# Kernel tuning notes

Measured on AMD Instinct MI355X. Metric: run time of the kernel, lower is better.

Reference implementation:

```python
import jax, jax.numpy as jnp
import numpy as np

B = 65536   # batch
HS = 8      # max hand size
E = 12      # card embed dim
A = 20      # max actions
KC = 4      # max cards per action (padded with 0)
NH, HD = 4, 3  # MHA heads, head dim (12/4)


def _xavier(k, out_dim, in_dim, gain):
    lim = gain * np.sqrt(6.0 / (in_dim + out_dim))
    return jax.random.uniform(k, (out_dim, in_dim), jnp.float32, -lim, lim)


def setup_inputs() -> dict:
    key = jax.random.key(0)
    ks = jax.random.split(key, 32)
    card_emb = 0.1 * jax.random.normal(ks[0], (54, E), jnp.float32)
    card_emb = card_emb.at[0].set(0.0)  # padding_idx=0
    enemy_emb = 0.1 * jax.random.normal(ks[1], (54, E), jnp.float32)
    enemy_emb = enemy_emb.at[0].set(0.0)
    inp = {
        'hand_cards': jax.random.randint(ks[2], (B, HS), 0, 54),
        'game_state': jax.random.normal(ks[3], (B, 12), jnp.float32),
        'discard_pile_cards': jax.random.uniform(ks[4], (B, 54), jnp.float32),
        'enemy_card': jax.random.randint(ks[5], (B, 1), 0, 54),
        'hand_size': jax.random.randint(ks[6], (B,), 1, HS + 1),
        'action_card_indices': jax.random.randint(ks[7], (A, KC), 0, 54),
        'num_valid_actions': 20,
        'card_emb': card_emb,
        'enemy_emb': enemy_emb,
        'in_w': _xavier(ks[8], 3 * E, E, 0.5),   # MHA in_proj (torch layout [3E,E])
        'in_b': jnp.zeros((3 * E,), jnp.float32),
        'out_w': _xavier(ks[9], E, E, 0.5),
        'out_b': jnp.zeros((E,), jnp.float32),
        'gs_w1': _xavier(ks[10], 64, 12, 0.8), 'gs_b1': jnp.zeros((64,)),
        'gs_w2': _xavier(ks[11], 6, 64, 0.8), 'gs_b2': jnp.zeros((6,)),
        'dp_w1': _xavier(ks[12], 64, 54, 0.8), 'dp_b1': jnp.zeros((64,)),
        'dp_w2': _xavier(ks[13], 6, 64, 0.8), 'dp_b2': jnp.zeros((6,)),
        'ctx_w1': _xavier(ks[14], 128, 36, 0.8), 'ctx_b1': jnp.zeros((128,)),
        'ctx_w2': _xavier(ks[15], 128, 128, 0.8), 'ctx_b2': jnp.zeros((128,)),
        'sc_w1': _xavier(ks[16], 32, 140, 0.8), 'sc_b1': jnp.zeros((32,)),
        'sc_w2': _xavier(ks[17], 1, 32, 0.8), 'sc_b2': jnp.zeros((1,)),
    }
    return inp


def reference(hand_cards, game_state, discard_pile_cards, enemy_card, hand_size,
              action_card_indices, num_valid_actions,
              card_emb, enemy_emb, in_w, in_b, out_w, out_b,
              gs_w1, gs_b1, gs_w2, gs_b2, dp_w1, dp_b1, dp_w2, dp_b2,
              ctx_w1, ctx_b1, ctx_w2, ctx_b2, sc_w1, sc_b1, sc_w2, sc_b2):
    b = hand_cards.shape[0]
    # hand embeddings + self-attention with key padding mask (card 0 = pad)
    he = card_emb[hand_cards]                                  # [B,8,12]
    mask = hand_cards != 0                                     # [B,8]
    qkv = he @ in_w.T + in_b                                   # [B,8,36]
    q, k, v = jnp.split(qkv, 3, axis=-1)
    hsplit = lambda t: t.reshape(b, HS, NH, HD)
    s = jnp.einsum('bqhd,bkhd->bhqk', hsplit(q), hsplit(k)) / np.sqrt(HD)
    s = jnp.where(mask[:, None, None, :], s, -1e9)
    attn = jax.nn.softmax(s, axis=-1)
    att = jnp.einsum('bhqk,bkhd->bqhd', attn, hsplit(v)).reshape(b, HS, E)
    att = att @ out_w.T + out_b                                # [B,8,12]
    lengths = jnp.maximum(hand_size.astype(jnp.float32), 1.0)[:, None]
    hand_ctx = att.sum(axis=1) / lengths                       # [B,12]
    # enemy / game-state / discard encoders (eval mode: dropout off)
    en = enemy_emb[enemy_card[:, 0]]                           # [B,12]
    g = jax.nn.relu(game_state @ gs_w1.T + gs_b1) @ gs_w2.T + gs_b2        # [B,6]
    d = jax.nn.relu(discard_pile_cards @ dp_w1.T + dp_b1) @ dp_w2.T + dp_b2  # [B,6]
    ctx = jnp.concatenate([hand_ctx, en, g, d], axis=-1)       # [B,36]
    ctx = jax.nn.relu(ctx @ ctx_w1.T + ctx_b1) @ ctx_w2.T + ctx_b2         # [B,128]
    # ragged per-action card lists: masked mean of card embeddings
    aemb = card_emb[action_card_indices]                       # [A,K,12]
    am = (action_card_indices != 0).astype(jnp.float32)[..., None]
    cnt = jnp.maximum(am.sum(axis=1), 1.0)
    arep = (aemb * am).sum(axis=1) / cnt                       # [A,12]
    feat = jnp.concatenate([
        jnp.broadcast_to(ctx[:, None, :], (b, A, ctx.shape[-1])),
        jnp.broadcast_to(arep[None], (b, A, E)),
    ], axis=-1)                                                # [B,A,140]
    sc = (jax.nn.relu(feat @ sc_w1.T + sc_b1) @ sc_w2.T + sc_b2)[..., 0]   # [B,A]
    valid = jnp.arange(A) < num_valid_actions
    return jnp.where(valid[None, :], sc, -1e8)
```

## Files before the change

kernel.cpp:

```cpp
#include <hip/hip_runtime.h>
#include <math.h>

#define HS 8
#define E 12
#define NA 20
#define KC 4

typedef float f32x4 __attribute__((ext_vector_type(4)));
typedef short short8 __attribute__((ext_vector_type(8)));

__device__ float g_ET[4 * 54 * 54];
__device__ float g_VT[4 * 54 * 4];
__device__ float g_abias[NA * 32];
__device__ float g_cb1f[128];
__device__ __align__(16) short g_gsB[4 * 64 * 16];
__device__ __align__(16) short g_dpB[8 * 64 * 16];
__device__ __align__(16) short g_ctxB2[40 * 64 * 16];
__device__ __align__(16) short g_WtB[8 * 64 * 16];
__device__ __align__(16) float g_feat[65536 * 32];

__device__ __forceinline__ void split_bf16(float f, short& hi, short& lo) {
    unsigned u = __float_as_uint(f);
    unsigned r = (u + 0x7FFFu + ((u >> 16) & 1u)) >> 16;
    hi = (short)r;
    float fh = __uint_as_float(r << 16);
    unsigned v = __float_as_uint(f - fh);
    unsigned r2 = (v + 0x7FFFu + ((v >> 16) & 1u)) >> 16;
    lo = (short)r2;
}

__device__ __forceinline__ void split8(const float* x, short8& hi, short8& lo) {
#pragma unroll
    for (int j = 0; j < 8; ++j) {
        short h, l;
        split_bf16(x[j], h, l);
        hi[j] = h; lo[j] = l;
    }
}

#define MFMA(a, b, c) __builtin_amdgcn_mfma_f32_16x16x32_bf16(a, b, c, 0, 0, 0)

__device__ __forceinline__ f32x4 mfma3(short8 ah, short8 al, const short* frag, f32x4 c) {
    const short8* bp = (const short8*)frag;
    short8 bh = bp[0], bl = bp[1];
    c = MFMA(ah, bh, c);
    c = MFMA(ah, bl, c);
    c = MFMA(al, bh, c);
    return c;
}

__device__ float wprime(int hid, int k, const float* ctx_w1, const float* out_w,
                        const float* out_b, const float* gs_w2, const float* dp_w2) {
    if (k < 12) {
        float s = 0.f;
        for (int i = 0; i < 12; ++i) s += ctx_w1[hid * 36 + i] * out_w[i * 12 + k];
        return s;
    } else if (k < 24) {
        return ctx_w1[hid * 36 + k];
    } else if (k == 24) {
        float s = 0.f;
        for (int i = 0; i < 12; ++i) s += ctx_w1[hid * 36 + i] * out_b[i];
        return 8.f * s;
    } else if (k < 32) {
        return 0.f;
    } else if (k < 96) {
        int u = k - 32;
        float s = 0.f;
        for (int c = 0; c < 6; ++c) s += ctx_w1[hid * 36 + 24 + c] * gs_w2[c * 64 + u];
        return s;
    } else {
        int u = k - 96;
        float s = 0.f;
        for (int c = 0; c < 6; ++c) s += ctx_w1[hid * 36 + 30 + c] * dp_w2[c * 64 + u];
        return s;
    }
}

__global__ void precompute_kernel(const float* __restrict__ card_emb,
                                  const int* __restrict__ aci,
                                  const float* __restrict__ ctx_w2,
                                  const float* __restrict__ ctx_b2,
                                  const float* __restrict__ sc_w1,
                                  const float* __restrict__ sc_b1,
                                  const float* __restrict__ in_w,
                                  const float* __restrict__ in_b,
                                  const float* __restrict__ ctx_w1,
                                  const float* __restrict__ ctx_b1,
                                  const float* __restrict__ dp_w1,
                                  const float* __restrict__ gs_w1,
                                  const float* __restrict__ gs_w2,
                                  const float* __restrict__ gs_b2,
                                  const float* __restrict__ dp_w2,
                                  const float* __restrict__ dp_b2,
                                  const float* __restrict__ out_w,
                                  const float* __restrict__ out_b) {
    const int O_ET = 11664, O_VT = O_ET + 216, O_GS = O_VT + 2048, O_DP = O_GS + 4096;
    const int O_CX = O_DP + 20480, O_WT = O_CX + 4096, O_AB = O_WT + 640, O_CB = O_AB + 128;
    int t = blockIdx.x * 256 + threadIdx.x;
    if (t < O_ET) {
        int h = t / 2916, rem = t % 2916;
        int c1 = rem / 54, c2 = rem % 54;
        float s = 0.f;
#pragma unroll
        for (int d = 0; d < 3; ++d) {
            float q = in_b[h * 3 + d], k = in_b[12 + h * 3 + d];
            for (int j = 0; j < 12; ++j) {
                q += in_w[(h * 3 + d) * 12 + j] * card_emb[c1 * 12 + j];
                k += in_w[(12 + h * 3 + d) * 12 + j] * card_emb[c2 * 12 + j];
            }
            s += q * k;
        }
        g_ET[t] = expf(s * 0.5773502691896258f);
    } else if (t < O_VT) {
        int t2 = t - O_ET;
        int h = t2 / 54, c = t2 % 54;
#pragma unroll
        for (int d = 0; d < 3; ++d) {
            float v = in_b[24 + h * 3 + d];
            for (int j = 0; j < 12; ++j)
                v += in_w[(24 + h * 3 + d) * 12 + j] * card_emb[c * 12 + j];
            g_VT[t2 * 4 + d] = v;
        }
        g_VT[t2 * 4 + 3] = 1.0f;
    } else if (t < O_GS) {
        int id = t - O_VT;
        int tt = id >> 9, lane = (id >> 3) & 63, j = id & 7;
        int g = lane >> 4, n = lane & 15;
        int k = 8 * g + j, col = 16 * tt + n;
        float wv = (k < 12) ? gs_w1[col * 12 + k] : 0.f;
        short hi, lo;
        split_bf16(wv, hi, lo);
        int base = ((tt << 6) + lane) << 4;
        g_gsB[base + j] = hi;
        g_gsB[base + 8 + j] = lo;
    } else if (t < O_DP) {
        int id = t - O_GS;
        int st = id >> 9, lane = (id >> 3) & 63, j = id & 7;
        int s = st >> 2, tt = st & 3;
        int g = lane >> 4, n = lane & 15;
        int k = 32 * s + 8 * g + j, col = 16 * tt + n;
        float wv = (k < 54) ? dp_w1[col * 54 + k] : 0.f;
        short hi, lo;
        split_bf16(wv, hi, lo);
        int base = ((st << 6) + lane) << 4;
        g_dpB[base + j] = hi;
        g_dpB[base + 8 + j] = lo;
    } else if (t < O_CX) {
        int id = t - O_DP;
        int st = id >> 9, lane = (id >> 3) & 63, j = id & 7;
        int s = st / 8, tt = st % 8;
        int g = lane >> 4, n = lane & 15;
        int k = 32 * s + 8 * g + j, col = 16 * tt + n;
        float wv = wprime(col, k, ctx_w1, out_w, out_b, gs_w2, dp_w2);
        short hi, lo;
        split_bf16(wv, hi, lo);
        int base = ((st << 6) + lane) << 4;
        g_ctxB2[base + j] = hi;
        g_ctxB2[base + 8 + j] = lo;
    } else if (t < O_WT) {
        int id = t - O_CX;
        int st = id >> 9, lane = (id >> 3) & 63, j = id & 7;
        int s = st >> 1, tt = st & 1;
        int g = lane >> 4, n = lane & 15;
        int k = 32 * s + 8 * g + j, col = 16 * tt + n;
        float wv = 0.f;
        for (int i = 0; i < 128; ++i) wv += sc_w1[col * 140 + i] * ctx_w2[i * 128 + k];
        short hi, lo;
        split_bf16(wv, hi, lo);
        int base = ((st << 6) + lane) << 4;
        g_WtB[base + j] = hi;
        g_WtB[base + 8 + j] = lo;
    } else if (t < O_AB) {
        int t2 = t - O_WT;
        int a = t2 >> 5, j = t2 & 31;
        float arep[E];
#pragma unroll
        for (int k2 = 0; k2 < E; ++k2) arep[k2] = 0.f;
        float cnt = 0.f;
#pragma unroll
        for (int c = 0; c < KC; ++c) {
            int idx = aci[a * KC + c];
            if (idx != 0) {
                cnt += 1.f;
#pragma unroll
                for (int k2 = 0; k2 < E; ++k2) arep[k2] += card_emb[idx * E + k2];
            }
        }
        float inv = 1.f / fmaxf(cnt, 1.f);
        float s = sc_b1[j];
#pragma unroll
        for (int k2 = 0; k2 < E; ++k2) s += sc_w1[j * 140 + 128 + k2] * (arep[k2] * inv);
        for (int i = 0; i < 128; ++i) s += sc_w1[j * 140 + i] * ctx_b2[i];
        g_abias[t2] = s;
    } else if (t < O_CB) {
        int hid = t - O_AB;
        float s = ctx_b1[hid];
        for (int c = 0; c < 6; ++c) {
            s += ctx_w1[hid * 36 + 24 + c] * gs_b2[c];
            s += ctx_w1[hid * 36 + 30 + c] * dp_b2[c];
        }
        g_cb1f[hid] = s;
    }
}

__global__ __launch_bounds__(1024) void featA_kernel(
    const int* __restrict__ hand_cards, const int* __restrict__ enemy_card,
    const int* __restrict__ hand_size, const float* __restrict__ enemy_emb) {
    __shared__ float sET[4 * 54 * 54];
    __shared__ __align__(16) float4 sV[4 * 54];
    __shared__ float sEN[54 * 12];

    int tid = threadIdx.x;
    for (int i = tid; i < 11664; i += 1024) sET[i] = g_ET[i];
    for (int i = tid; i < 864; i += 1024) ((float*)sV)[i] = g_VT[i];
    for (int i = tid; i < 648; i += 1024) sEN[i] = enemy_emb[i];
    __syncthreads();

    int q = tid & 3;
    int el = tid >> 2;
    int b = blockIdx.x * 256 + el;

    int hc[HS];
    {
        const int4* hp = (const int4*)(hand_cards + (size_t)b * HS);
        int4 h0 = hp[0], h1 = hp[1];
        hc[0] = h0.x; hc[1] = h0.y; hc[2] = h0.z; hc[3] = h0.w;
        hc[4] = h1.x; hc[5] = h1.y; hc[6] = h1.z; hc[7] = h1.w;
    }
    int ec = enemy_card[b];

    float4 vv[HS];
#pragma unroll
    for (int k = 0; k < HS; ++k) {
        float4 v = sV[q * 54 + hc[k]];
        if (hc[k] == 0) v = make_float4(0.f, 0.f, 0.f, 0.f);
        vv[k] = v;
    }

    const float* eb = sET + q * 2916;
    float a0 = 0.f, a1 = 0.f, a2 = 0.f;
#pragma unroll
    for (int p = 0; p < HS; ++p) {
        const float* er = eb + hc[p] * 54;
        float n0 = 0.f, n1 = 0.f, n2 = 0.f, nw = 0.f;
#pragma unroll
        for (int k = 0; k < HS; ++k) {
            float e = er[hc[k]];
            n0 += e * vv[k].x;
            n1 += e * vv[k].y;
            n2 += e * vv[k].z;
            nw += e * vv[k].w;
        }
        float rw = 1.f / fmaxf(nw, 1e-30f);
        a0 += n0 * rw; a1 += n1 * rw; a2 += n2 * rw;
    }
    float invlen = 1.f / fmaxf((float)hand_size[b], 1.f);
    float* fr = g_feat + (size_t)b * 32;
    fr[3 * q + 0] = a0 * invlen;
    fr[3 * q + 1] = a1 * invlen;
    fr[3 * q + 2] = a2 * invlen;
    fr[12 + 3 * q + 0] = sEN[ec * 12 + 3 * q + 0];
    fr[12 + 3 * q + 1] = sEN[ec * 12 + 3 * q + 1];
    fr[12 + 3 * q + 2] = sEN[ec * 12 + 3 * q + 2];
    if (q == 0) fr[24] = invlen;
}

#define FENCE() do { asm volatile("s_waitcnt lgkmcnt(0)" ::: "memory"); \
                     __builtin_amdgcn_sched_barrier(0); } while (0)

__global__ __launch_bounds__(256) void scoreB_kernel(
    const float* __restrict__ game_state, const float* __restrict__ discard,
    const int* __restrict__ num_valid, const float* __restrict__ gs_b1,
    const float* __restrict__ dp_b1, const float* __restrict__ sc_w2,
    const float* __restrict__ sc_b2, float* __restrict__ out) {
    __shared__ __align__(16) float sA[4 * 16 * 132];
    __shared__ __align__(16) float sAB[NA * 36];
    __shared__ __align__(16) float sW2[32];
    __shared__ float sCB[128];
    __shared__ float sGSB[64];
    __shared__ float sDPB[64];

    int tid = threadIdx.x;
    for (int i = tid; i < NA * 36; i += 256) {
        int a = i / 36, c = i % 36;
        sAB[i] = (c < 32) ? g_abias[a * 32 + c] : 0.f;
    }
    if (tid >= 160 && tid < 192) sW2[tid - 160] = sc_w2[tid - 160];
    if (tid < 128) sCB[tid] = g_cb1f[tid];
    if (tid >= 192 && tid < 256) sGSB[tid - 192] = gs_b1[tid - 192];
    if (tid >= 128 && tid < 160) { sDPB[tid - 128] = dp_b1[tid - 128]; sDPB[tid - 96] = dp_b1[tid - 96]; }
    __syncthreads();

    int lane = tid & 63;
    int w = tid >> 6;
    int n = lane & 15, g = lane >> 4;
    size_t b2 = (size_t)blockIdx.x * 64 + (w << 4) + n;
    float* SA = sA + w * 2112;

    {
        float xg[8];
#pragma unroll
        for (int j = 0; j < 8; ++j) {
            int k = 8 * g + j;
            xg[j] = (k < 12) ? game_state[b2 * 12 + k] : 0.f;
        }
        short8 xh, xl;
        split8(xg, xh, xl);
        f32x4 gacc[4];
#pragma unroll
        for (int t = 0; t < 4; ++t) {
            float bv = sGSB[16 * t + n];
            f32x4 cc = {bv, bv, bv, bv};
            gacc[t] = mfma3(xh, xl, &g_gsB[((t << 6) + lane) << 4], cc);
        }
#pragma unroll
        for (int t = 0; t < 4; ++t)
#pragma unroll
            for (int r = 0; r < 4; ++r)
                SA[(4 * g + r) * 132 + 16 * t + n] = fmaxf(gacc[t][r], 0.f);
    }
    {
        const float* drow = discard + b2 * 54;
        float xa[8], xb[8];
        {
            const float2* p = (const float2*)(drow + 8 * g);
            float2 v0 = p[0], v1 = p[1], v2 = p[2], v3 = p[3];
            xa[0] = v0.x; xa[1] = v0.y; xa[2] = v1.x; xa[3] = v1.y;
            xa[4] = v2.x; xa[5] = v2.y; xa[6] = v3.x; xa[7] = v3.y;
        }
#pragma unroll
        for (int j = 0; j < 8; ++j) {
            int k = 32 + 8 * g + j;
            xb[j] = (k < 54) ? drow[k] : 0.f;
        }
        short8 ah0, al0, ah1, al1;
        split8(xa, ah0, al0);
        split8(xb, ah1, al1);
        f32x4 dacc[4];
#pragma unroll
        for (int t = 0; t < 4; ++t) {
            float bv = sDPB[16 * t + n];
            f32x4 cc = {bv, bv, bv, bv};
            cc = mfma3(ah0, al0, &g_dpB[((t << 6) + lane) << 4], cc);
            cc = mfma3(ah1, al1, &g_dpB[(((4 + t) << 6) + lane) << 4], cc);
            dacc[t] = cc;
        }
#pragma unroll
        for (int t = 0; t < 4; ++t)
#pragma unroll
            for (int r = 0; r < 4; ++r)
                SA[(4 * g + r) * 132 + 64 + 16 * t + n] = fmaxf(dacc[t][r], 0.f);
    }
    FENCE();

    f32x4 cacc[8];
#pragma unroll
    for (int tt = 0; tt < 8; ++tt) {
        float bv = sCB[16 * tt + n];
        f32x4 cc = {bv, bv, bv, bv};
        cacc[tt] = cc;
    }
    {
        const float4* fp = (const float4*)(g_feat + b2 * 32 + 8 * g);
        float4 f0 = fp[0], f1 = fp[1];
        float ca[8] = {f0.x, f0.y, f0.z, f0.w, f1.x, f1.y, f1.z, f1.w};
        short8 ah, al;
        split8(ca, ah, al);
#pragma unroll
        for (int tt = 0; tt < 8; ++tt)
            cacc[tt] = mfma3(ah, al, &g_ctxB2[((tt << 6) + lane) << 4], cacc[tt]);
    }
#pragma unroll
    for (int s = 1; s < 5; ++s) {
        const float4* ap = (const float4*)&SA[n * 132 + 32 * (s - 1) + 8 * g];
        float4 a0 = ap[0], a1 = ap[1];
        float ca[8] = {a0.x, a0.y, a0.z, a0.w, a1.x, a1.y, a1.z, a1.w};
        short8 ah, al;
        split8(ca, ah, al);
#pragma unroll
        for (int tt = 0; tt < 8; ++tt)
            cacc[tt] = mfma3(ah, al, &g_ctxB2[(((s * 8 + tt) << 6) + lane) << 4], cacc[tt]);
    }
    FENCE();
#pragma unroll
    for (int tt = 0; tt < 8; ++tt)
#pragma unroll
        for (int r = 0; r < 4; ++r)
            SA[(4 * g + r) * 132 + 16 * tt + n] = fmaxf(cacc[tt][r], 0.f);
    FENCE();

    f32x4 uacc[2];
    {
        f32x4 z = {0.f, 0.f, 0.f, 0.f};
        uacc[0] = z; uacc[1] = z;
    }
#pragma unroll
    for (int s = 0; s < 4; ++s) {
        const float4* ap = (const float4*)&SA[n * 132 + 32 * s + 8 * g];
        float4 a0 = ap[0], a1 = ap[1];
        float ha[8] = {a0.x, a0.y, a0.z, a0.w, a1.x, a1.y, a1.z, a1.w};
        short8 ah, al;
        split8(ha, ah, al);
#pragma unroll
        for (int t2 = 0; t2 < 2; ++t2)
            uacc[t2] = mfma3(ah, al, &g_WtB[(((s * 2 + t2) << 6) + lane) << 4], uacc[t2]);
    }
    FENCE();
#pragma unroll
    for (int t2 = 0; t2 < 2; ++t2)
#pragma unroll
        for (int r = 0; r < 4; ++r)
            SA[(4 * g + r) * 132 + 16 * t2 + n] = uacc[t2][r];
    FENCE();

    {
        float uu[32];
        {
            const float4* up = (const float4*)&SA[n * 132];
#pragma unroll
            for (int j8 = 0; j8 < 8; ++j8) {
                float4 v = up[j8];
                uu[4 * j8 + 0] = v.x; uu[4 * j8 + 1] = v.y;
                uu[4 * j8 + 2] = v.z; uu[4 * j8 + 3] = v.w;
            }
        }
        int nva = num_valid[0];
        float sb2 = sc_b2[0];
#pragma unroll
        for (int t = 0; t < 5; ++t) {
            int a = g * 5 + t;
            const float4* ab = (const float4*)&sAB[a * 36];
            float s = sb2;
#pragma unroll
            for (int j8 = 0; j8 < 8; ++j8) {
                float4 av = ab[j8];
                float4 wv = ((const float4*)sW2)[j8];
                s += wv.x * fmaxf(uu[4 * j8 + 0] + av.x, 0.f);
                s += wv.y * fmaxf(uu[4 * j8 + 1] + av.y, 0.f);
                s += wv.z * fmaxf(uu[4 * j8 + 2] + av.z, 0.f);
                s += wv.w * fmaxf(uu[4 * j8 + 3] + av.w, 0.f);
            }
            out[b2 * NA + a] = (a < nva) ? s : -1.0e8f;
        }
    }
}

extern "C" void kernel_launch(void* const* d_in, const int* in_sizes, int n_in,
                              void* d_out, int out_size, void* d_ws, size_t ws_size,
                              hipStream_t stream) {
    const int* hand_cards = (const int*)d_in[0];
    const float* game_state = (const float*)d_in[1];
    const float* discard = (const float*)d_in[2];
    const int* enemy_card = (const int*)d_in[3];
    const int* hand_size = (const int*)d_in[4];
    const int* aci = (const int*)d_in[5];
    const int* num_valid = (const int*)d_in[6];
    const float* card_emb = (const float*)d_in[7];
    const float* enemy_emb = (const float*)d_in[8];
    const float* in_w = (const float*)d_in[9];
    const float* in_b = (const float*)d_in[10];
    const float* out_w = (const float*)d_in[11];
    const float* out_b = (const float*)d_in[12];
    const float* gs_w1 = (const float*)d_in[13];
    const float* gs_b1 = (const float*)d_in[14];
    const float* gs_w2 = (const float*)d_in[15];
    const float* gs_b2 = (const float*)d_in[16];
    const float* dp_w1 = (const float*)d_in[17];
    const float* dp_b1 = (const float*)d_in[18];
    const float* dp_w2 = (const float*)d_in[19];
    const float* dp_b2 = (const float*)d_in[20];
    const float* ctx_w1 = (const float*)d_in[21];
    const float* ctx_b1 = (const float*)d_in[22];
    const float* ctx_w2 = (const float*)d_in[23];
    const float* ctx_b2 = (const float*)d_in[24];
    const float* sc_w1 = (const float*)d_in[25];
    const float* sc_b1 = (const float*)d_in[26];
    const float* sc_w2 = (const float*)d_in[27];
    const float* sc_b2 = (const float*)d_in[28];

    int B = in_sizes[0] / HS;

    precompute_kernel<<<170, 256, 0, stream>>>(
        card_emb, aci, ctx_w2, ctx_b2, sc_w1, sc_b1, in_w, in_b, ctx_w1, ctx_b1,
        dp_w1, gs_w1, gs_w2, gs_b2, dp_w2, dp_b2, out_w, out_b);
    featA_kernel<<<B / 256, 1024, 0, stream>>>(hand_cards, enemy_card, hand_size,
                                               enemy_emb);
    scoreB_kernel<<<B / 64, 256, 0, stream>>>(game_state, discard, num_valid,
                                              gs_b1, dp_b1, sc_w2, sc_b2,
                                              (float*)d_out);
}
```

Baseline: 56.97 us.

## Unfold gs/dp second layers, process two row tiles per wave in scoreB

Stops folding gs_w2/dp_w2 into the ctx first-layer weights, which was a 160-wide K dimension. Instead the 64→6 projections are computed explicitly with FMAs plus cross-lane shuffles, shrinking the ctx MFMA input to K=64. Each wave now handles 32 rows (two 16-row tiles), so every B-fragment load is reused across both tiles. The grid is halved to compensate. bf16 splitting switches to the library conversion intrinsic. The cost is more registers and LDS per block, plus extra shuffle work.

```diff
diff --git a/kernel.cpp b/kernel.cpp
--- a/kernel.cpp
+++ b/kernel.cpp
@@ -1,4 +1,5 @@
 #include <hip/hip_runtime.h>
+#include <hip/hip_bf16.h>
 #include <math.h>
 
 #define HS 8
@@ -12,23 +13,20 @@
 __device__ float g_ET[4 * 54 * 54];
 __device__ float g_VT[4 * 54 * 4];
 __device__ float g_abias[NA * 32];
-__device__ float g_cb1f[128];
 __device__ __align__(16) short g_gsB[4 * 64 * 16];
 __device__ __align__(16) short g_dpB[8 * 64 * 16];
-__device__ __align__(16) short g_ctxB2[40 * 64 * 16];
+__device__ __align__(16) short g_ctxB[16 * 64 * 16];
 __device__ __align__(16) short g_WtB[8 * 64 * 16];
 __device__ __align__(16) float g_feat[65536 * 32];
 
+__device__ __forceinline__ short bfh(float f) {
+    return (short)__bfloat16_as_ushort(__float2bfloat16(f));
+}
 __device__ __forceinline__ void split_bf16(float f, short& hi, short& lo) {
-    unsigned u = __float_as_uint(f);
-    unsigned r = (u + 0x7FFFu + ((u >> 16) & 1u)) >> 16;
-    hi = (short)r;
-    float fh = __uint_as_float(r << 16);
-    unsigned v = __float_as_uint(f - fh);
-    unsigned r2 = (v + 0x7FFFu + ((v >> 16) & 1u)) >> 16;
-    lo = (short)r2;
-}
-
+    hi = bfh(f);
+    float fh = __uint_as_float(((unsigned)(unsigned short)hi) << 16);
+    lo = bfh(f - fh);
+}
 __device__ __forceinline__ void split8(const float* x, short8& hi, short8& lo) {
 #pragma unroll
     for (int j = 0; j < 8; ++j) {
@@ -40,17 +38,16 @@
 
 #define MFMA(a, b, c) __builtin_amdgcn_mfma_f32_16x16x32_bf16(a, b, c, 0, 0, 0)
 
-__device__ __forceinline__ f32x4 mfma3(short8 ah, short8 al, const short* frag, f32x4 c) {
-    const short8* bp = (const short8*)frag;
-    short8 bh = bp[0], bl = bp[1];
+__device__ __forceinline__ f32x4 mfma3v(short8 ah, short8 al, short8 bh, short8 bl,
+                                        f32x4 c) {
     c = MFMA(ah, bh, c);
     c = MFMA(ah, bl, c);
     c = MFMA(al, bh, c);
     return c;
 }
 
-__device__ float wprime(int hid, int k, const float* ctx_w1, const float* out_w,
-                        const float* out_b, const float* gs_w2, const float* dp_w2) {
+__device__ float ctxw(int hid, int k, const float* ctx_w1, const float* out_w,
+                      const float* out_b) {
     if (k < 12) {
         float s = 0.f;
         for (int i = 0; i < 12; ++i) s += ctx_w1[hid * 36 + i] * out_w[i * 12 + k];
@@ -63,17 +60,10 @@
         return 8.f * s;
     } else if (k < 32) {
         return 0.f;
-    } else if (k < 96) {
-        int u = k - 32;
-        float s = 0.f;
-        for (int c = 0; c < 6; ++c) s += ctx_w1[hid * 36 + 24 + c] * gs_w2[c * 64 + u];
-        return s;
-    } else {
-        int u = k - 96;
-        float s = 0.f;
-        for (int c = 0; c < 6; ++c) s += ctx_w1[hid * 36 + 30 + c] * dp_w2[c * 64 + u];
-        return s;
-    }
+    } else if (k < 44) {
+        return ctx_w1[hid * 36 + 24 + (k - 32)];
+    }
+    return 0.f;
 }
 
 __global__ void precompute_kernel(const float* __restrict__ card_emb,
@@ -85,17 +75,12 @@
                                   const float* __restrict__ in_w,
                                   const float* __restrict__ in_b,
                                   const float* __restrict__ ctx_w1,
-                                  const float* __restrict__ ctx_b1,
                                   const float* __restrict__ dp_w1,
                                   const float* __restrict__ gs_w1,
-                                  const float* __restrict__ gs_w2,
-                                  const float* __restrict__ gs_b2,
-                                  const float* __restrict__ dp_w2,
-                                  const float* __restrict__ dp_b2,
                                   const float* __restrict__ out_w,
                                   const float* __restrict__ out_b) {
     const int O_ET = 11664, O_VT = O_ET + 216, O_GS = O_VT + 2048, O_DP = O_GS + 4096;
-    const int O_CX = O_DP + 20480, O_WT = O_CX + 4096, O_AB = O_WT + 640, O_CB = O_AB + 128;
+    const int O_CX = O_DP + 8192, O_WT = O_CX + 4096, O_AB = O_WT + 640;
     int t = blockIdx.x * 256 + threadIdx.x;
     if (t < O_ET) {
         int h = t / 2916, rem = t % 2916;
@@ -148,15 +133,15 @@
     } else if (t < O_CX) {
         int id = t - O_DP;
         int st = id >> 9, lane = (id >> 3) & 63, j = id & 7;
-        int s = st / 8, tt = st % 8;
+        int s = st >> 3, tt = st & 7;
         int g = lane >> 4, n = lane & 15;
-        int k = 32 * s + 8 * g + j, col = 16 * tt + n;
-        float wv = wprime(col, k, ctx_w1, out_w, out_b, gs_w2, dp_w2);
+        int k = 32 * s + 8 * g + j, hid = 16 * tt + n;
+        float wv = ctxw(hid, k, ctx_w1, out_w, out_b);
         short hi, lo;
         split_bf16(wv, hi, lo);
         int base = ((st << 6) + lane) << 4;
-        g_ctxB2[base + j] = hi;
-        g_ctxB2[base + 8 + j] = lo;
+        g_ctxB[base + j] = hi;
+        g_ctxB[base + 8 + j] = lo;
     } else if (t < O_WT) {
         int id = t - O_CX;
         int st = id >> 9, lane = (id >> 3) & 63, j = id & 7;
@@ -192,14 +177,6 @@
         for (int k2 = 0; k2 < E; ++k2) s += sc_w1[j * 140 + 128 + k2] * (arep[k2] * inv);
         for (int i = 0; i < 128; ++i) s += sc_w1[j * 140 + i] * ctx_b2[i];
         g_abias[t2] = s;
-    } else if (t < O_CB) {
-        int hid = t - O_AB;
-        float s = ctx_b1[hid];
-        for (int c = 0; c < 6; ++c) {
-            s += ctx_w1[hid * 36 + 24 + c] * gs_b2[c];
-            s += ctx_w1[hid * 36 + 30 + c] * dp_b2[c];
-        }
-        g_cb1f[hid] = s;
     }
 }
 
@@ -271,11 +248,16 @@
 __global__ __launch_bounds__(256) void scoreB_kernel(
     const float* __restrict__ game_state, const float* __restrict__ discard,
     const int* __restrict__ num_valid, const float* __restrict__ gs_b1,
-    const float* __restrict__ dp_b1, const float* __restrict__ sc_w2,
-    const float* __restrict__ sc_b2, float* __restrict__ out) {
-    __shared__ __align__(16) float sA[4 * 16 * 132];
+    const float* __restrict__ dp_b1, const float* __restrict__ gs_w2,
+    const float* __restrict__ dp_w2, const float* __restrict__ gs_b2,
+    const float* __restrict__ dp_b2, const float* __restrict__ ctx_b1,
+    const float* __restrict__ sc_w2, const float* __restrict__ sc_b2,
+    float* __restrict__ out) {
+    __shared__ __align__(16) float sU[4 * 4224];
     __shared__ __align__(16) float sAB[NA * 36];
     __shared__ __align__(16) float sW2[32];
+    __shared__ __align__(16) float sGS2T[64 * 12];
+    __shared__ __align__(16) float sDPW2T[64 * 12];
     __shared__ float sCB[128];
     __shared__ float sGSB[64];
     __shared__ float sDPB[64];
@@ -285,138 +267,253 @@
         int a = i / 36, c = i % 36;
         sAB[i] = (c < 32) ? g_abias[a * 32 + c] : 0.f;
     }
-    if (tid >= 160 && tid < 192) sW2[tid - 160] = sc_w2[tid - 160];
-    if (tid < 128) sCB[tid] = g_cb1f[tid];
-    if (tid >= 192 && tid < 256) sGSB[tid - 192] = gs_b1[tid - 192];
-    if (tid >= 128 && tid < 160) { sDPB[tid - 128] = dp_b1[tid - 128]; sDPB[tid - 96] = dp_b1[tid - 96]; }
+    for (int i = tid; i < 768; i += 256) {
+        int r = i / 12, c = i % 12;
+        sGS2T[i] = (c < 6) ? gs_w2[c * 64 + r] : 0.f;
+        sDPW2T[i] = (c < 6) ? dp_w2[c * 64 + r] : 0.f;
+    }
+    if (tid < 32) sW2[tid] = sc_w2[tid];
+    if (tid >= 32 && tid < 160) sCB[tid - 32] = ctx_b1[tid - 32];
+    if (tid >= 160 && tid < 224) sGSB[tid - 160] = gs_b1[tid - 160];
+    if (tid >= 192 && tid < 256) sDPB[tid - 192] = dp_b1[tid - 192];
+    for (int i = tid; i < 4 * 640; i += 256) {
+        int w2 = i / 640;
+        sU[w2 * 4224 + (i % 640)] = 0.f;
+    }
     __syncthreads();
 
     int lane = tid & 63;
     int w = tid >> 6;
     int n = lane & 15, g = lane >> 4;
-    size_t b2 = (size_t)blockIdx.x * 64 + (w << 4) + n;
-    float* SA = sA + w * 2112;
-
+    size_t eb0 = (size_t)blockIdx.x * 128 + (w << 5);
+    float* SW = sU + w * 4224;
+    float gb2 = (n < 6) ? gs_b2[n] : 0.f;
+    float db2 = (n < 6) ? dp_b2[n] : 0.f;
+
+    f32x4 gacc[2][4], dacc[2][4];
     {
-        float xg[8];
-#pragma unroll
-        for (int j = 0; j < 8; ++j) {
-            int k = 8 * g + j;
-            xg[j] = (k < 12) ? game_state[b2 * 12 + k] : 0.f;
-        }
-        short8 xh, xl;
-        split8(xg, xh, xl);
-        f32x4 gacc[4];
+        short8 gah[2], gal[2], dah0[2], dal0[2], dah1[2], dal1[2];
+#pragma unroll
+        for (int tau = 0; tau < 2; ++tau) {
+            size_t bE = eb0 + 16 * tau + n;
+            float xg[8];
+#pragma unroll
+            for (int j = 0; j < 8; ++j) {
+                int k = 8 * g + j;
+                xg[j] = (k < 12) ? game_state[bE * 12 + k] : 0.f;
+            }
+            split8(xg, gah[tau], gal[tau]);
+            const float* drow = discard + bE * 54;
+            float xa[8], xb[8];
+            {
+                const float2* p = (const float2*)(drow + 8 * g);
+                float2 v0 = p[0], v1 = p[1], v2 = p[2], v3 = p[3];
+                xa[0] = v0.x; xa[1] = v0.y; xa[2] = v1.x; xa[3] = v1.y;
+                xa[4] = v2.x; xa[5] = v2.y; xa[6] = v3.x; xa[7] = v3.y;
+            }
+#pragma unroll
+            for (int j = 0; j < 8; ++j) {
+                int k = 32 + 8 * g + j;
+                xb[j] = (k < 54) ? drow[k] : 0.f;
+            }
+            split8(xa, dah0[tau], dal0[tau]);
+            split8(xb, dah1[tau], dal1[tau]);
+        }
 #pragma unroll
         for (int t = 0; t < 4; ++t) {
+            const short8* bp = (const short8*)&g_gsB[((t << 6) + lane) << 4];
+            short8 bh = bp[0], bl = bp[1];
             float bv = sGSB[16 * t + n];
-            f32x4 cc = {bv, bv, bv, bv};
-            gacc[t] = mfma3(xh, xl, &g_gsB[((t << 6) + lane) << 4], cc);
-        }
-#pragma unroll
-        for (int t = 0; t < 4; ++t)
-#pragma unroll
-            for (int r = 0; r < 4; ++r)
-                SA[(4 * g + r) * 132 + 16 * t + n] = fmaxf(gacc[t][r], 0.f);
-    }
-    {
-        const float* drow = discard + b2 * 54;
-        float xa[8], xb[8];
-        {
-            const float2* p = (const float2*)(drow + 8 * g);
-            float2 v0 = p[0], v1 = p[1], v2 = p[2], v3 = p[3];
-            xa[0] = v0.x; xa[1] = v0.y; xa[2] = v1.x; xa[3] = v1.y;
-            xa[4] = v2.x; xa[5] = v2.y; xa[6] = v3.x; xa[7] = v3.y;
-        }
-#pragma unroll
-        for (int j = 0; j < 8; ++j) {
-            int k = 32 + 8 * g + j;
-            xb[j] = (k < 54) ? drow[k] : 0.f;
-        }
-        short8 ah0, al0, ah1, al1;
-        split8(xa, ah0, al0);
-        split8(xb, ah1, al1);
-        f32x4 dacc[4];
+#pragma unroll
+            for (int tau = 0; tau < 2; ++tau) {
+                f32x4 cc = {bv, bv, bv, bv};
+                gacc[tau][t] = mfma3v(gah[tau], gal[tau], bh, bl, cc);
+            }
+        }
 #pragma unroll
         for (int t = 0; t < 4; ++t) {
+            const short8* b0 = (const short8*)&g_dpB[((t << 6) + lane) << 4];
+            short8 b0h = b0[0], b0l = b0[1];
+            const short8* b1 = (const short8*)&g_dpB[(((4 + t) << 6) + lane) << 4];
+            short8 b1h = b1[0], b1l = b1[1];
             float bv = sDPB[16 * t + n];
-            f32x4 cc = {bv, bv, bv, bv};
-            cc = mfma3(ah0, al0, &g_dpB[((t << 6) + lane) << 4], cc);
-            cc = mfma3(ah1, al1, &g_dpB[(((4 + t) << 6) + lane) << 4], cc);
-            dacc[t] = cc;
-        }
-#pragma unroll
-        for (int t = 0; t < 4; ++t)
-#pragma unroll
-            for (int r = 0; r < 4; ++r)
-                SA[(4 * g + r) * 132 + 64 + 16 * t + n] = fmaxf(dacc[t][r], 0.f);
+#pragma unroll
+            for (int tau = 0; tau < 2; ++tau) {
+                f32x4 cc = {bv, bv, bv, bv};
+                cc = mfma3v(dah0[tau], dal0[tau], b0h, b0l, cc);
+                dacc[tau][t] = mfma3v(dah1[tau], dal1[tau], b1h, b1l, cc);
+            }
+        }
+    }
+
+#pragma unroll
+    for (int tau = 0; tau < 2; ++tau) {
+        float pg[4][6], pd[4][6];
+#pragma unroll
+        for (int r = 0; r < 4; ++r)
+#pragma unroll
+            for (int c = 0; c < 6; ++c) { pg[r][c] = 0.f; pd[r][c] = 0.f; }
+#pragma unroll
+        for (int t = 0; t < 4; ++t) {
+            const float* wg = &sGS2T[(16 * t + n) * 12];
+            float4 wga = *(const float4*)wg;
+            float2 wgb = *(const float2*)(wg + 4);
+            const float* wd = &sDPW2T[(16 * t + n) * 12];
+            float4 wda = *(const float4*)wd;
+            float2 wdb = *(const float2*)(wd + 4);
+#pragma unroll
+            for (int r = 0; r < 4; ++r) {
+                float hg = fmaxf(gacc[tau][t][r], 0.f);
+                float hd = fmaxf(dacc[tau][t][r], 0.f);
+                pg[r][0] += hg * wga.x; pg[r][1] += hg * wga.y; pg[r][2] += hg * wga.z;
+                pg[r][3] += hg * wga.w; pg[r][4] += hg * wgb.x; pg[r][5] += hg * wgb.y;
+                pd[r][0] += hd * wda.x; pd[r][1] += hd * wda.y; pd[r][2] += hd * wda.z;
+                pd[r][3] += hd * wda.w; pd[r][4] += hd * wdb.x; pd[r][5] += hd * wdb.y;
+            }
+        }
+#pragma unroll
+        for (int r = 0; r < 4; ++r)
+#pragma unroll
+            for (int c = 0; c < 6; ++c) {
+                float v = pg[r][c];
+                v += __shfl_xor(v, 1, 64);
+                v += __shfl_xor(v, 2, 64);
+                v += __shfl_xor(v, 4, 64);
+                v += __shfl_xor(v, 8, 64);
+                pg[r][c] = v;
+                float u = pd[r][c];
+                u += __shfl_xor(u, 1, 64);
+                u += __shfl_xor(u, 2, 64);
+                u += __shfl_xor(u, 4, 64);
+                u += __shfl_xor(u, 8, 64);
+                pd[r][c] = u;
+            }
+        if (n < 6) {
+#pragma unroll
+            for (int r = 0; r < 4; ++r) {
+                int e = 16 * tau + 4 * g + r;
+                float gv = pg[r][0];
+                gv = (n == 1) ? pg[r][1] : gv; gv = (n == 2) ? pg[r][2] : gv;
+                gv = (n == 3) ? pg[r][3] : gv; gv = (n == 4) ? pg[r][4] : gv;
+                gv = (n == 5) ? pg[r][5] : gv;
+                float dv = pd[r][0];
+                dv = (n == 1) ? pd[r][1] : dv; dv = (n == 2) ? pd[r][2] : dv;
+                dv = (n == 3) ? pd[r][3] : dv; dv = (n == 4) ? pd[r][4] : dv;
+                dv = (n == 5) ? pd[r][5] : dv;
+                SW[e * 20 + n] = gv + gb2;
+                SW[e * 20 + 6 + n] = dv + db2;
+            }
+        }
     }
     FENCE();
 
-    f32x4 cacc[8];
+    f32x4 cacc[2][8];
 #pragma unroll
     for (int tt = 0; tt < 8; ++tt) {
         float bv = sCB[16 * tt + n];
-        f32x4 cc = {bv, bv, bv, bv};
-        cacc[tt] = cc;
+#pragma unroll
+        for (int tau = 0; tau < 2; ++tau) {
+            f32x4 cc = {bv, bv, bv, bv};
+            cacc[tau][tt] = cc;
+        }
     }
     {
-        const float4* fp = (const float4*)(g_feat + b2 * 32 + 8 * g);
-        float4 f0 = fp[0], f1 = fp[1];
-        float ca[8] = {f0.x, f0.y, f0.z, f0.w, f1.x, f1.y, f1.z, f1.w};
-        short8 ah, al;
-        split8(ca, ah, al);
+        short8 ah[2], al[2];
+#pragma unroll
+        for (int tau = 0; tau < 2; ++tau) {
+            size_t bE = eb0 + 16 * tau + n;
+            const float4* fp = (const float4*)(g_feat + bE * 32 + 8 * g);
+            float4 f0 = fp[0], f1 = fp[1];
+            float ca[8] = {f0.x, f0.y, f0.z, f0.w, f1.x, f1.y, f1.z, f1.w};
+            split8(ca, ah[tau], al[tau]);
+        }
+#pragma unroll
+        for (int tt = 0; tt < 8; ++tt) {
+            const short8* bp = (const short8*)&g_ctxB[((tt << 6) + lane) << 4];
+            short8 bh = bp[0], bl = bp[1];
+#pragma unroll
+            for (int tau = 0; tau < 2; ++tau)
+                cacc[tau][tt] = mfma3v(ah[tau], al[tau], bh, bl, cacc[tau][tt]);
+        }
+#pragma unroll
+        for (int tau = 0; tau < 2; ++tau) {
+            if (g < 2) {
+                int e = 16 * tau + n;
+                float xb[8];
+#pragma unroll
+                for (int j2 = 0; j2 < 4; ++j2) {
+                    float2 v = *(const float2*)&SW[e * 20 + 8 * g + 2 * j2];
+                    xb[2 * j2] = v.x;
+                    xb[2 * j2 + 1] = v.y;
+                }
+                split8(xb, ah[tau], al[tau]);
+            } else {
+                short8 zz = {0, 0, 0, 0, 0, 0, 0, 0};
+                ah[tau] = zz; al[tau] = zz;
+            }
+        }
+#pragma unroll
+        for (int tt = 0; tt < 8; ++tt) {
+            const short8* bp = (const short8*)&g_ctxB[(((8 + tt) << 6) + lane) << 4];
+            short8 bh = bp[0], bl = bp[1];
+#pragma unroll
+            for (int tau = 0; tau < 2; ++tau)
+                cacc[tau][tt] = mfma3v(ah[tau], al[tau], bh, bl, cacc[tau][tt]);
+        }
+    }
+    FENCE();
+
+#pragma unroll
+    for (int tau = 0; tau < 2; ++tau)
 #pragma unroll
         for (int tt = 0; tt < 8; ++tt)
-            cacc[tt] = mfma3(ah, al, &g_ctxB2[((tt << 6) + lane) << 4], cacc[tt]);
-    }
-#pragma unroll
-    for (int s = 1; s < 5; ++s) {
-        const float4* ap = (const float4*)&SA[n * 132 + 32 * (s - 1) + 8 * g];
-        float4 a0 = ap[0], a1 = ap[1];
-        float ca[8] = {a0.x, a0.y, a0.z, a0.w, a1.x, a1.y, a1.z, a1.w};
-        short8 ah, al;
-        split8(ca, ah, al);
-#pragma unroll
-        for (int tt = 0; tt < 8; ++tt)
-            cacc[tt] = mfma3(ah, al, &g_ctxB2[(((s * 8 + tt) << 6) + lane) << 4], cacc[tt]);
-    }
+#pragma unroll
+            for (int r = 0; r < 4; ++r)
+                SW[(16 * tau + 4 * g + r) * 132 + 16 * tt + n] =
+                    fmaxf(cacc[tau][tt][r], 0.f);
     FENCE();
-#pragma unroll
-    for (int tt = 0; tt < 8; ++tt)
-#pragma unroll
-        for (int r = 0; r < 4; ++r)
-            SA[(4 * g + r) * 132 + 16 * tt + n] = fmaxf(cacc[tt][r], 0.f);
-    FENCE();
-
-    f32x4 uacc[2];
+
+    f32x4 uacc[2][2];
     {
         f32x4 z = {0.f, 0.f, 0.f, 0.f};
-        uacc[0] = z; uacc[1] = z;
+        uacc[0][0] = z; uacc[0][1] = z; uacc[1][0] = z; uacc[1][1] = z;
     }
 #pragma unroll
     for (int s = 0; s < 4; ++s) {
-        const float4* ap = (const float4*)&SA[n * 132 + 32 * s + 8 * g];
-        float4 a0 = ap[0], a1 = ap[1];
-        float ha[8] = {a0.x, a0.y, a0.z, a0.w, a1.x, a1.y, a1.z, a1.w};
-        short8 ah, al;
-        split8(ha, ah, al);
+        short8 ah[2], al[2];
+#pragma unroll
+        for (int tau = 0; tau < 2; ++tau) {
+            const float4* ap = (const float4*)&SW[(16 * tau + n) * 132 + 32 * s + 8 * g];
+            float4 a0 = ap[0], a1 = ap[1];
+            float ha[8] = {a0.x, a0.y, a0.z, a0.w, a1.x, a1.y, a1.z, a1.w};
+            split8(ha, ah[tau], al[tau]);
+        }
+#pragma unroll
+        for (int t2 = 0; t2 < 2; ++t2) {
+            const short8* bp = (const short8*)&g_WtB[(((s * 2 + t2) << 6) + lane) << 4];
+            short8 bh = bp[0], bl = bp[1];
+#pragma unroll
+            for (int tau = 0; tau < 2; ++tau)
+                uacc[tau][t2] = mfma3v(ah[tau], al[tau], bh, bl, uacc[tau][t2]);
+        }
+    }
+    FENCE();
+
+#pragma unroll
+    for (int tau = 0; tau < 2; ++tau)
 #pragma unroll
         for (int t2 = 0; t2 < 2; ++t2)
-            uacc[t2] = mfma3(ah, al, &g_WtB[(((s * 2 + t2) << 6) + lane) << 4], uacc[t2]);
-    }
+#pragma unroll
+            for (int r = 0; r < 4; ++r)
+                SW[(16 * tau + 4 * g + r) * 132 + 16 * t2 + n] = uacc[tau][t2][r];
     FENCE();
-#pragma unroll
-    for (int t2 = 0; t2 < 2; ++t2)
-#pragma unroll
-        for (int r = 0; r < 4; ++r)
-            SA[(4 * g + r) * 132 + 16 * t2 + n] = uacc[t2][r];
-    FENCE();
-
-    {
+    int nva = num_valid[0];
+    float sb2 = sc_b2[0];
+#pragma unroll
+    for (int tau = 0; tau < 2; ++tau) {
         float uu[32];
         {
-            const float4* up = (const float4*)&SA[n * 132];
+            const float4* up = (const float4*)&SW[(16 * tau + n) * 132];
 #pragma unroll
             for (int j8 = 0; j8 < 8; ++j8) {
                 float4 v = up[j8];
@@ -424,8 +521,7 @@
                 uu[4 * j8 + 2] = v.z; uu[4 * j8 + 3] = v.w;
             }
         }
-        int nva = num_valid[0];
-        float sb2 = sc_b2[0];
+        size_t bE = eb0 + 16 * tau + n;
 #pragma unroll
         for (int t = 0; t < 5; ++t) {
             int a = g * 5 + t;
@@ -440,7 +536,7 @@
                 s += wv.z * fmaxf(uu[4 * j8 + 2] + av.z, 0.f);
                 s += wv.w * fmaxf(uu[4 * j8 + 3] + av.w, 0.f);
             }
-            out[b2 * NA + a] = (a < nva) ? s : -1.0e8f;
+            out[bE * NA + a] = (a < nva) ? s : -1.0e8f;
         }
     }
 }
@@ -480,12 +576,12 @@
 
     int B = in_sizes[0] / HS;
 
-    precompute_kernel<<<170, 256, 0, stream>>>(
-        card_emb, aci, ctx_w2, ctx_b2, sc_w1, sc_b1, in_w, in_b, ctx_w1, ctx_b1,
-        dp_w1, gs_w1, gs_w2, gs_b2, dp_w2, dp_b2, out_w, out_b);
+    precompute_kernel<<<121, 256, 0, stream>>>(
+        card_emb, aci, ctx_w2, ctx_b2, sc_w1, sc_b1, in_w, in_b, ctx_w1,
+        dp_w1, gs_w1, out_w, out_b);
     featA_kernel<<<B / 256, 1024, 0, stream>>>(hand_cards, enemy_card, hand_size,
                                                enemy_emb);
-    scoreB_kernel<<<B / 64, 256, 0, stream>>>(game_state, discard, num_valid,
-                                              gs_b1, dp_b1, sc_w2, sc_b2,
-                                              (float*)d_out);
-}
+    scoreB_kernel<<<B / 128, 256, 0, stream>>>(
+        game_state, discard, num_valid, gs_b1, dp_b1, gs_w2, dp_w2, gs_b2, dp_b2,
+        ctx_b1, sc_w2, sc_b2, (float*)d_out);
+}
```

Result: slower. 74.17 us (+30.2%).

## Split fused scoring kernel into three GEMM kernels with global bf16 intermediates

Applied to the files above, without the earlier changes.

Breaks the single fused scoreB kernel into gemmA (game-state and discard first layers), gemmB (context layer 1) and gemmC (final projection and scoring). The intermediate activations are written to large transposed global buffers as packed hi/lo bf16 pairs. Each kernel stages its weight fragments in shared memory instead of reading them from global. This is meant to cut per-block LDS pressure and improve weight reuse, at the cost of two extra launches and roughly 64MB of extra global write and read traffic per intermediate buffer.

```diff
diff --git a/kernel.cpp b/kernel.cpp
--- a/kernel.cpp
+++ b/kernel.cpp
@@ -1,4 +1,5 @@
 #include <hip/hip_runtime.h>
+#include <hip/hip_bf16.h>
 #include <math.h>
 
 #define HS 8
@@ -18,17 +19,17 @@
 __device__ __align__(16) short g_ctxB2[40 * 64 * 16];
 __device__ __align__(16) short g_WtB[8 * 64 * 16];
 __device__ __align__(16) float g_feat[65536 * 32];
-
+__device__ __align__(16) unsigned g_h1T[128 * 65536];
+__device__ __align__(16) unsigned g_h2T[128 * 65536];
+
+__device__ __forceinline__ short bfh(float f) {
+    return (short)__bfloat16_as_ushort(__float2bfloat16(f));
+}
 __device__ __forceinline__ void split_bf16(float f, short& hi, short& lo) {
-    unsigned u = __float_as_uint(f);
-    unsigned r = (u + 0x7FFFu + ((u >> 16) & 1u)) >> 16;
-    hi = (short)r;
-    float fh = __uint_as_float(r << 16);
-    unsigned v = __float_as_uint(f - fh);
-    unsigned r2 = (v + 0x7FFFu + ((v >> 16) & 1u)) >> 16;
-    lo = (short)r2;
-}
-
+    hi = bfh(f);
+    float fh = __uint_as_float(((unsigned)(unsigned short)hi) << 16);
+    lo = bfh(f - fh);
+}
 __device__ __forceinline__ void split8(const float* x, short8& hi, short8& lo) {
 #pragma unroll
     for (int j = 0; j < 8; ++j) {
@@ -37,12 +38,16 @@
         hi[j] = h; lo[j] = l;
     }
 }
+__device__ __forceinline__ unsigned packsp(float f) {
+    short h, l;
+    split_bf16(f, h, l);
+    return (((unsigned)(unsigned short)h) << 16) | (unsigned)(unsigned short)l;
+}
 
 #define MFMA(a, b, c) __builtin_amdgcn_mfma_f32_16x16x32_bf16(a, b, c, 0, 0, 0)
 
-__device__ __forceinline__ f32x4 mfma3(short8 ah, short8 al, const short* frag, f32x4 c) {
-    const short8* bp = (const short8*)frag;
-    short8 bh = bp[0], bl = bp[1];
+__device__ __forceinline__ f32x4 mfma3v(short8 ah, short8 al, short8 bh, short8 bl,
+                                        f32x4 c) {
     c = MFMA(ah, bh, c);
     c = MFMA(ah, bl, c);
     c = MFMA(al, bh, c);
@@ -150,8 +155,8 @@
         int st = id >> 9, lane = (id >> 3) & 63, j = id & 7;
         int s = st / 8, tt = st % 8;
         int g = lane >> 4, n = lane & 15;
-        int k = 32 * s + 8 * g + j, col = 16 * tt + n;
-        float wv = wprime(col, k, ctx_w1, out_w, out_b, gs_w2, dp_w2);
+        int k = 32 * s + 8 * g + j, hid = 16 * tt + n;
+        float wv = wprime(hid, k, ctx_w1, out_w, out_b, gs_w2, dp_w2);
         short hi, lo;
         split_bf16(wv, hi, lo);
         int base = ((st << 6) + lane) << 4;
@@ -265,62 +270,37 @@
     if (q == 0) fr[24] = invlen;
 }
 
-#define FENCE() do { asm volatile("s_waitcnt lgkmcnt(0)" ::: "memory"); \
-                     __builtin_amdgcn_sched_barrier(0); } while (0)
-
-__global__ __launch_bounds__(256) void scoreB_kernel(
+#define FENCE() asm volatile("s_waitcnt lgkmcnt(0)" ::: "memory")
+
+__global__ __launch_bounds__(256) void gemmA_kernel(
     const float* __restrict__ game_state, const float* __restrict__ discard,
-    const int* __restrict__ num_valid, const float* __restrict__ gs_b1,
-    const float* __restrict__ dp_b1, const float* __restrict__ sc_w2,
-    const float* __restrict__ sc_b2, float* __restrict__ out) {
-    __shared__ __align__(16) float sA[4 * 16 * 132];
-    __shared__ __align__(16) float sAB[NA * 36];
-    __shared__ __align__(16) float sW2[32];
-    __shared__ float sCB[128];
-    __shared__ float sGSB[64];
-    __shared__ float sDPB[64];
+    const float* __restrict__ gs_b1, const float* __restrict__ dp_b1) {
+    __shared__ __align__(16) short sGs[4 * 64 * 16];
+    __shared__ __align__(16) short sDp[8 * 64 * 16];
+    __shared__ float sGSB[64], sDPB[64];
 
     int tid = threadIdx.x;
-    for (int i = tid; i < NA * 36; i += 256) {
-        int a = i / 36, c = i % 36;
-        sAB[i] = (c < 32) ? g_abias[a * 32 + c] : 0.f;
-    }
-    if (tid >= 160 && tid < 192) sW2[tid - 160] = sc_w2[tid - 160];
-    if (tid < 128) sCB[tid] = g_cb1f[tid];
-    if (tid >= 192 && tid < 256) sGSB[tid - 192] = gs_b1[tid - 192];
-    if (tid >= 128 && tid < 160) { sDPB[tid - 128] = dp_b1[tid - 128]; sDPB[tid - 96] = dp_b1[tid - 96]; }
+    for (int i = tid; i < 512; i += 256) ((int4*)sGs)[i] = ((const int4*)g_gsB)[i];
+    for (int i = tid; i < 1024; i += 256) ((int4*)sDp)[i] = ((const int4*)g_dpB)[i];
+    if (tid < 64) sGSB[tid] = gs_b1[tid];
+    if (tid >= 64 && tid < 128) sDPB[tid - 64] = dp_b1[tid - 64];
     __syncthreads();
 
     int lane = tid & 63;
-    int w = tid >> 6;
     int n = lane & 15, g = lane >> 4;
-    size_t b2 = (size_t)blockIdx.x * 64 + (w << 4) + n;
-    float* SA = sA + w * 2112;
-
+    size_t eb = (size_t)blockIdx.x * 64 + ((tid >> 6) << 4);
+    size_t bE = eb + n;
+
+    short8 gah, gal, dah0, dal0, dah1, dal1;
     {
         float xg[8];
 #pragma unroll
         for (int j = 0; j < 8; ++j) {
             int k = 8 * g + j;
-            xg[j] = (k < 12) ? game_state[b2 * 12 + k] : 0.f;
-        }
-        short8 xh, xl;
-        split8(xg, xh, xl);
-        f32x4 gacc[4];
-#pragma unroll
-        for (int t = 0; t < 4; ++t) {
-            float bv = sGSB[16 * t + n];
-            f32x4 cc = {bv, bv, bv, bv};
-            gacc[t] = mfma3(xh, xl, &g_gsB[((t << 6) + lane) << 4], cc);
-        }
-#pragma unroll
-        for (int t = 0; t < 4; ++t)
-#pragma unroll
-            for (int r = 0; r < 4; ++r)
-                SA[(4 * g + r) * 132 + 16 * t + n] = fmaxf(gacc[t][r], 0.f);
-    }
-    {
-        const float* drow = discard + b2 * 54;
+            xg[j] = (k < 12) ? game_state[bE * 12 + k] : 0.f;
+        }
+        split8(xg, gah, gal);
+        const float* drow = discard + bE * 54;
         float xa[8], xb[8];
         {
             const float2* p = (const float2*)(drow + 8 * g);
@@ -333,61 +313,128 @@
             int k = 32 + 8 * g + j;
             xb[j] = (k < 54) ? drow[k] : 0.f;
         }
-        short8 ah0, al0, ah1, al1;
-        split8(xa, ah0, al0);
-        split8(xb, ah1, al1);
-        f32x4 dacc[4];
-#pragma unroll
-        for (int t = 0; t < 4; ++t) {
-            float bv = sDPB[16 * t + n];
+        split8(xa, dah0, dal0);
+        split8(xb, dah1, dal1);
+    }
+#pragma unroll
+    for (int tt = 0; tt < 4; ++tt) {
+        const short8* bp = (const short8*)&sGs[((tt << 6) + lane) << 4];
+        float bv = sGSB[16 * tt + n];
+        f32x4 cc = {bv, bv, bv, bv};
+        cc = mfma3v(gah, gal, bp[0], bp[1], cc);
+        uint4 v;
+        v.x = packsp(fmaxf(cc[0], 0.f));
+        v.y = packsp(fmaxf(cc[1], 0.f));
+        v.z = packsp(fmaxf(cc[2], 0.f));
+        v.w = packsp(fmaxf(cc[3], 0.f));
+        *(uint4*)(g_h1T + (size_t)(16 * tt + n) * 65536 + eb + 4 * g) = v;
+    }
+#pragma unroll
+    for (int tt = 0; tt < 4; ++tt) {
+        const short8* b0 = (const short8*)&sDp[((tt << 6) + lane) << 4];
+        const short8* b1 = (const short8*)&sDp[(((4 + tt) << 6) + lane) << 4];
+        float bv = sDPB[16 * tt + n];
+        f32x4 cc = {bv, bv, bv, bv};
+        cc = mfma3v(dah0, dal0, b0[0], b0[1], cc);
+        cc = mfma3v(dah1, dal1, b1[0], b1[1], cc);
+        uint4 v;
+        v.x = packsp(fmaxf(cc[0], 0.f));
+        v.y = packsp(fmaxf(cc[1], 0.f));
+        v.z = packsp(fmaxf(cc[2], 0.f));
+        v.w = packsp(fmaxf(cc[3], 0.f));
+        *(uint4*)(g_h1T + (size_t)(64 + 16 * tt + n) * 65536 + eb + 4 * g) = v;
+    }
+}
+
+__global__ __launch_bounds__(256) void gemmB_kernel() {
+    __shared__ __align__(16) short sCx[40 * 64 * 16];
+    __shared__ float sCB[128];
+
+    int tid = threadIdx.x;
+    for (int i = tid; i < 5120; i += 256) ((int4*)sCx)[i] = ((const int4*)g_ctxB2)[i];
+    if (tid < 128) sCB[tid] = g_cb1f[tid];
+    __syncthreads();
+
+    int lane = tid & 63;
+    int n = lane & 15, g = lane >> 4;
+    size_t base = (size_t)blockIdx.x * 256 + ((tid >> 6) << 6);
+
+#pragma unroll
+    for (int t = 0; t < 4; ++t) {
+        size_t eb = base + t * 16;
+        size_t bE = eb + n;
+        f32x4 cacc[8];
+#pragma unroll
+        for (int tt = 0; tt < 8; ++tt) {
+            float bv = sCB[16 * tt + n];
             f32x4 cc = {bv, bv, bv, bv};
-            cc = mfma3(ah0, al0, &g_dpB[((t << 6) + lane) << 4], cc);
-            cc = mfma3(ah1, al1, &g_dpB[(((4 + t) << 6) + lane) << 4], cc);
-            dacc[t] = cc;
-        }
-#pragma unroll
-        for (int t = 0; t < 4; ++t)
-#pragma unroll
-            for (int r = 0; r < 4; ++r)
-                SA[(4 * g + r) * 132 + 64 + 16 * t + n] = fmaxf(dacc[t][r], 0.f);
-    }
-    FENCE();
-
-    f32x4 cacc[8];
-#pragma unroll
-    for (int tt = 0; tt < 8; ++tt) {
-        float bv = sCB[16 * tt + n];
-        f32x4 cc = {bv, bv, bv, bv};
-        cacc[tt] = cc;
-    }
-    {
-        const float4* fp = (const float4*)(g_feat + b2 * 32 + 8 * g);
-        float4 f0 = fp[0], f1 = fp[1];
-        float ca[8] = {f0.x, f0.y, f0.z, f0.w, f1.x, f1.y, f1.z, f1.w};
-        short8 ah, al;
-        split8(ca, ah, al);
-#pragma unroll
-        for (int tt = 0; tt < 8; ++tt)
-            cacc[tt] = mfma3(ah, al, &g_ctxB2[((tt << 6) + lane) << 4], cacc[tt]);
-    }
-#pragma unroll
-    for (int s = 1; s < 5; ++s) {
-        const float4* ap = (const float4*)&SA[n * 132 + 32 * (s - 1) + 8 * g];
-        float4 a0 = ap[0], a1 = ap[1];
-        float ca[8] = {a0.x, a0.y, a0.z, a0.w, a1.x, a1.y, a1.z, a1.w};
-        short8 ah, al;
-        split8(ca, ah, al);
-#pragma unroll
-        for (int tt = 0; tt < 8; ++tt)
-            cacc[tt] = mfma3(ah, al, &g_ctxB2[(((s * 8 + tt) << 6) + lane) << 4], cacc[tt]);
-    }
-    FENCE();
-#pragma unroll
-    for (int tt = 0; tt < 8; ++tt)
-#pragma unroll
-        for (int r = 0; r < 4; ++r)
-            SA[(4 * g + r) * 132 + 16 * tt + n] = fmaxf(cacc[tt][r], 0.f);
-    FENCE();
+            cacc[tt] = cc;
+        }
+        {
+            const float4* fp = (const float4*)(g_feat + bE * 32 + 8 * g);
+            float4 f0 = fp[0], f1 = fp[1];
+            float fx[8] = {f0.x, f0.y, f0.z, f0.w, f1.x, f1.y, f1.z, f1.w};
+            short8 ah, al;
+            split8(fx, ah, al);
+#pragma unroll
+            for (int tt = 0; tt < 8; ++tt) {
+                const short8* bp = (const short8*)&sCx[((tt << 6) + lane) << 4];
+                cacc[tt] = mfma3v(ah, al, bp[0], bp[1], cacc[tt]);
+            }
+        }
+#pragma unroll
+        for (int s = 1; s < 5; ++s) {
+            unsigned va[8];
+#pragma unroll
+            for (int j = 0; j < 8; ++j)
+                va[j] = g_h1T[(size_t)((s - 1) * 32 + 8 * g + j) * 65536 + bE];
+            short8 ah, al;
+#pragma unroll
+            for (int j = 0; j < 8; ++j) {
+                ah[j] = (short)(va[j] >> 16);
+                al[j] = (short)(va[j] & 0xffffu);
+            }
+#pragma unroll
+            for (int tt = 0; tt < 8; ++tt) {
+                const short8* bp = (const short8*)&sCx[(((s * 8 + tt) << 6) + lane) << 4];
+                cacc[tt] = mfma3v(ah, al, bp[0], bp[1], cacc[tt]);
+            }
+        }
+#pragma unroll
+        for (int tt = 0; tt < 8; ++tt) {
+            uint4 v;
+            v.x = packsp(fmaxf(cacc[tt][0], 0.f));
+            v.y = packsp(fmaxf(cacc[tt][1], 0.f));
+            v.z = packsp(fmaxf(cacc[tt][2], 0.f));
+            v.w = packsp(fmaxf(cacc[tt][3], 0.f));
+            *(uint4*)(g_h2T + (size_t)(16 * tt + n) * 65536 + eb + 4 * g) = v;
+        }
+    }
+}
+
+__global__ __launch_bounds__(256) void gemmC_kernel(
+    const int* __restrict__ num_valid, const float* __restrict__ sc_w2,
+    const float* __restrict__ sc_b2, float* __restrict__ out) {
+    __shared__ __align__(16) short sWt[8 * 64 * 16];
+    __shared__ __align__(16) float sAB[NA * 36];
+    __shared__ __align__(16) float sW2[32];
+    __shared__ __align__(16) float sT[4 * 16 * 36];
+
+    int tid = threadIdx.x;
+    for (int i = tid; i < 1024; i += 256) ((int4*)sWt)[i] = ((const int4*)g_WtB)[i];
+    for (int i = tid; i < NA * 36; i += 256) {
+        int a = i / 36, c = i % 36;
+        sAB[i] = (c < 32) ? g_abias[a * 32 + c] : 0.f;
+    }
+    if (tid < 32) sW2[tid] = sc_w2[tid];
+    __syncthreads();
+
+    int lane = tid & 63;
+    int w = tid >> 6;
+    int n = lane & 15, g = lane >> 4;
+    size_t eb = (size_t)blockIdx.x * 64 + (w << 4);
+    size_t bE = eb + n;
+    float* SW = sT + w * 576;
 
     f32x4 uacc[2];
     {
@@ -396,27 +443,32 @@
     }
 #pragma unroll
     for (int s = 0; s < 4; ++s) {
-        const float4* ap = (const float4*)&SA[n * 132 + 32 * s + 8 * g];
-        float4 a0 = ap[0], a1 = ap[1];
-        float ha[8] = {a0.x, a0.y, a0.z, a0.w, a1.x, a1.y, a1.z, a1.w};
+        unsigned va[8];
+#pragma unroll
+        for (int j = 0; j < 8; ++j)
+            va[j] = g_h2T[(size_t)(32 * s + 8 * g + j) * 65536 + bE];
         short8 ah, al;
-        split8(ha, ah, al);
-#pragma unroll
-        for (int t2 = 0; t2 < 2; ++t2)
-            uacc[t2] = mfma3(ah, al, &g_WtB[(((s * 2 + t2) << 6) + lane) << 4], uacc[t2]);
-    }
+#pragma unroll
+        for (int j = 0; j < 8; ++j) {
+            ah[j] = (short)(va[j] >> 16);
+            al[j] = (short)(va[j] & 0xffffu);
+        }
+#pragma unroll
+        for (int t2 = 0; t2 < 2; ++t2) {
+            const short8* bp = (const short8*)&sWt[(((s * 2 + t2) << 6) + lane) << 4];
+            uacc[t2] = mfma3v(ah, al, bp[0], bp[1], uacc[t2]);
+        }
+    }
+#pragma unroll
+    for (int t2 = 0; t2 < 2; ++t2)
+#pragma unroll
+        for (int r = 0; r < 4; ++r)
+            SW[(4 * g + r) * 36 + 16 * t2 + n] = uacc[t2][r];
     FENCE();
-#pragma unroll
-    for (int t2 = 0; t2 < 2; ++t2)
-#pragma unroll
-        for (int r = 0; r < 4; ++r)
-            SA[(4 * g + r) * 132 + 16 * t2 + n] = uacc[t2][r];
-    FENCE();
-
     {
         float uu[32];
         {
-            const float4* up = (const float4*)&SA[n * 132];
+            const float4* up = (const float4*)&SW[n * 36];
 #pragma unroll
             for (int j8 = 0; j8 < 8; ++j8) {
                 float4 v = up[j8];
@@ -440,7 +492,7 @@
                 s += wv.z * fmaxf(uu[4 * j8 + 2] + av.z, 0.f);
                 s += wv.w * fmaxf(uu[4 * j8 + 3] + av.w, 0.f);
             }
-            out[b2 * NA + a] = (a < nva) ? s : -1.0e8f;
+            out[bE * NA + a] = (a < nva) ? s : -1.0e8f;
         }
     }
 }
@@ -485,7 +537,7 @@
         dp_w1, gs_w1, gs_w2, gs_b2, dp_w2, dp_b2, out_w, out_b);
     featA_kernel<<<B / 256, 1024, 0, stream>>>(hand_cards, enemy_card, hand_size,
                                                enemy_emb);
-    scoreB_kernel<<<B / 64, 256, 0, stream>>>(game_state, discard, num_valid,
-                                              gs_b1, dp_b1, sc_w2, sc_b2,
-                                              (float*)d_out);
-}
+    gemmA_kernel<<<B / 64, 256, 0, stream>>>(game_state, discard, gs_b1, dp_b1);
+    gemmB_kernel<<<B / 256, 256, 0, stream>>>();
+    gemmC_kernel<<<B / 64, 256, 0, stream>>>(num_valid, sc_w2, sc_b2, (float*)d_out);
+}
```

Result: slower. 89.81 us (+57.7%).
